# Kernel tuning notes

Hardware: AMD Instinct MI355X
Metric: run time of the kernel (lower is better)

## Reference

```python
import jax, jax.numpy as jnp
import numpy as np

EPS = float(np.finfo(np.float64).eps)


def _gat(x, src, dst, W, a_src, a_dst, b, N):
    # PyG GATConv, heads=1, concat=False, eval (no dropout). Self-loops already in src/dst.
    h = x @ W                              # [N, C]
    al = (h * a_src).sum(-1)               # [N] alpha_src per node
    ar = (h * a_dst).sum(-1)               # [N] alpha_dst per node
    e = jax.nn.leaky_relu(al[src] + ar[dst], 0.2)   # [E]
    m = jax.ops.segment_max(e, dst, num_segments=N)
    ee = jnp.exp(e - m[dst])
    s = jax.ops.segment_sum(ee, dst, num_segments=N)
    alpha = ee / (s[dst] + 1e-16)          # edge softmax grouped by dst
    return jax.ops.segment_sum(alpha[:, None] * h[src], dst, num_segments=N) + b


def setup_inputs() -> dict:
    key = jax.random.key(0)
    N, F, H, C, G, E = 10000, 128, 64, 2, 4, 320000
    ks = jax.random.split(key, 12)
    x = jax.random.normal(ks[0], (N, F), jnp.float32)
    y = jax.random.randint(ks[1], (N,), 0, 2)
    train_mask = jax.random.randint(ks[2], (N,), 0, 2).astype(jnp.int32)
    edge_ppi = jax.random.randint(ks[3], (2, E), 0, N)
    edge_hom = jax.random.randint(ks[4], (2, E), 0, N)
    g = lambda k, s, fan: jax.random.normal(k, s, jnp.float32) * (1.0 / np.sqrt(fan))
    W1 = g(ks[5], (G, F, H), F)
    a_src1 = g(ks[6], (G, H), H)
    a_dst1 = g(ks[7], (G, H), H)
    b1 = jnp.zeros((G, H), jnp.float32)
    gamma = jnp.ones((G, H), jnp.float32)
    beta = jnp.zeros((G, H), jnp.float32)
    W2 = g(ks[8], (G, H, C), H)
    a_src2 = g(ks[9], (G, C), C)
    a_dst2 = g(ks[10], (G, C), C)
    b2 = jnp.zeros((G, C), jnp.float32)
    emb_w = jnp.zeros((F,), jnp.float32)    # nn.Parameter init zeros
    logit_p = jnp.zeros((F,), jnp.float32)  # ConcreteDropout init zeros
    return dict(x=x, y=y, train_mask=train_mask, edge_ppi=edge_ppi, edge_hom=edge_hom,
                W1=W1, a_src1=a_src1, a_dst1=a_dst1, b1=b1, gamma=gamma, beta=beta,
                W2=W2, a_src2=a_src2, a_dst2=a_dst2, b2=b2, emb_w=emb_w, logit_p=logit_p)


def reference(x, y, train_mask, edge_ppi, edge_hom, W1, a_src1, a_dst1, b1,
              gamma, beta, W2, a_src2, a_dst2, b2, emb_w, logit_p):
    N = x.shape[0]
    G = W1.shape[0]
    loop = jnp.arange(N)
    sl = jnp.stack([loop, loop])
    ei_p = jnp.concatenate([edge_ppi, sl], axis=1)  # add self-loops (PyG default)
    ei_h = jnp.concatenate([edge_hom, sl], axis=1)
    mask = (train_mask > 0).astype(x.dtype)
    out = jnp.zeros((N,), x.dtype)
    loss = jnp.zeros((1,), x.dtype)
    for i in range(G):  # fixed small number of GAT branches
        ei = ei_p if i % 2 == 0 else ei_h
        src, dst = ei[0], ei[1]
        hid = _gat(x, src, dst, W1[i], a_src1[i], a_dst1[i], b1[i], N)
        hid = hid * gamma[i] / jnp.sqrt(1.0 + 1e-5) + beta[i]  # BN eval, init stats
        hid = jax.nn.leaky_relu(hid, 0.01)
        o = _gat(hid, src, dst, W2[i], a_src2[i], a_dst2[i], b2[i], N)
        logp = jax.nn.log_softmax(o, axis=1)
        pick = jnp.take_along_axis(logp, y[:, None], axis=1)[:, 0]
        loss = loss + (-(mask * pick).sum() / mask.sum())  # nll_loss on train_mask
        out = out + jnp.exp(logp[:, 1])
    node_p = out / G
    # GeneralizationGraph (eval: unif_noise = 0.5)
    p = jax.nn.sigmoid(logit_p)
    approx = (jnp.log(p + EPS) - jnp.log(1.0 - p + EPS)
              + jnp.log(0.5 + EPS) - jnp.log(0.5 + EPS))
    keep = 1.0 - jax.nn.sigmoid(approx / 0.1)
    emb = x * keep
    pw = 1.0 - p
    ex = emb * jax.nn.sigmoid(emb_w)
    graph = (ex @ ex.T) / (ex.sum(1) + 1e-6)  # [N,N]; column j scaled by 1/rowsum_j
    npc = node_p[:, None]
    adj = graph @ npc
    adj_n = graph @ (1.0 - npc)
    norm = jax.nn.softmax(jnp.concatenate([adj_n, adj], axis=1), axis=1)
    return (node_p, loss / G, norm[:, 1], graph, pw)
```

## Files before the change

### kernel.cpp

```cpp
#include <hip/hip_runtime.h>
#include <hip/hip_bf16.h>
#include <math.h>

#define N_NODES 10000
#define FDIM 128
#define HDIM 64
#define NEDGES 320000
#define M_EDGES (NEDGES + N_NODES)

typedef __attribute__((ext_vector_type(8))) short short8;
typedef __attribute__((ext_vector_type(4))) float floatx4;

__device__ __forceinline__ float lrelu(float v, float s){ return v >= 0.f ? v : s*v; }

__global__ void k_count(const int* __restrict__ ep, const int* __restrict__ eh,
                        int* __restrict__ ptr_p, int* __restrict__ ptr_h){
  int idx = blockIdx.x*blockDim.x + threadIdx.x;
  if (idx >= 2*M_EDGES) return;
  int list = idx >= M_EDGES;
  int e = idx - list*M_EDGES;
  const int* el = list ? eh : ep;
  int* ptr = list ? ptr_h : ptr_p;
  int dst = (e < NEDGES) ? el[NEDGES + e] : (e - NEDGES);
  atomicAdd(&ptr[dst+1], 1);
}

__global__ void k_scan(int* __restrict__ ptr_p, int* __restrict__ cur_p,
                       int* __restrict__ ptr_h, int* __restrict__ cur_h){
  __shared__ int wsum[4];
  __shared__ int carry;
  int t = threadIdx.x, wid = t>>6, lane = t&63;
  for (int a = 0; a < 2; ++a){
    int* ptr = a ? ptr_h : ptr_p;
    int* cur = a ? cur_h : cur_p;
    if (t == 0) carry = 0;
    __syncthreads();
    for (int base = 0; base <= N_NODES; base += 256){
      int i = base + t;
      int v = (i <= N_NODES) ? ptr[i] : 0;
      int sc = v;
      #pragma unroll
      for (int off=1; off<64; off<<=1){ int u = __shfl_up(sc, off); if (lane >= off) sc += u; }
      if (lane == 63) wsum[wid] = sc;
      __syncthreads();
      int wo = 0;
      for (int w = 0; w < wid; ++w) wo += wsum[w];
      int val = carry + wo + sc;
      if (i <= N_NODES) ptr[i] = val;
      if (i <  N_NODES) cur[i] = val;
      __syncthreads();
      if (t == 0) carry += wsum[0]+wsum[1]+wsum[2]+wsum[3];
      __syncthreads();
    }
  }
}

__global__ void k_fill(const int* __restrict__ ep, const int* __restrict__ eh,
                       int* __restrict__ cur_p, int* __restrict__ cur_h,
                       int* __restrict__ src_p, int* __restrict__ src_h){
  int idx = blockIdx.x*blockDim.x + threadIdx.x;
  if (idx >= 2*M_EDGES) return;
  int list = idx >= M_EDGES;
  int e = idx - list*M_EDGES;
  const int* el = list ? eh : ep;
  int* cur  = list ? cur_h : cur_p;
  int* sarr = list ? src_h : src_p;
  int src, dst;
  if (e < NEDGES){ src = el[e]; dst = el[NEDGES+e]; } else { src = dst = e - NEDGES; }
  int pos = atomicAdd(&cur[dst], 1);
  sarr[pos] = src;
}

__global__ void k_masksum(const int* __restrict__ tm, float* __restrict__ misc){
  __shared__ int ssum[4];
  int idx = blockIdx.x*blockDim.x + threadIdx.x;
  int c = 0;
  for (int i = idx; i < N_NODES; i += gridDim.x*blockDim.x) c += (tm[i] > 0);
  #pragma unroll
  for (int off=32; off; off>>=1) c += __shfl_down(c, off);
  if ((threadIdx.x & 63) == 0) ssum[threadIdx.x>>6] = c;
  __syncthreads();
  if (threadIdx.x == 0) atomicAdd(&misc[1], (float)(ssum[0]+ssum[1]+ssum[2]+ssum[3]));
}

__global__ __launch_bounds__(256) void k_gemm1(const float* __restrict__ x, const float* __restrict__ W1,
    const float* __restrict__ asrc, const float* __restrict__ adst,
    float* __restrict__ h, float* __restrict__ al, float* __restrict__ ar){
  int wid = threadIdx.x>>6, lane = threadIdx.x&63;
  int r = blockIdx.x*4 + wid;
  if (r >= N_NODES) return;
  const float* xr = x + (size_t)r*FDIM;
  float xv0 = xr[lane], xv1 = xr[64+lane];
  float acc = 0.f;
  #pragma unroll 16
  for (int k=0;k<64;k++) acc = fmaf(__shfl(xv0,k), W1[k*HDIM+lane], acc);
  #pragma unroll 16
  for (int k=0;k<64;k++) acc = fmaf(__shfl(xv1,k), W1[(64+k)*HDIM+lane], acc);
  h[(size_t)r*HDIM + lane] = acc;
  float pa = acc*asrc[lane], pb = acc*adst[lane];
  #pragma unroll
  for (int off=32; off; off>>=1){ pa += __shfl_down(pa,off); pb += __shfl_down(pb,off); }
  if (lane==0){ al[r]=pa; ar[r]=pb; }
}

__global__ __launch_bounds__(256) void k_gat1(const int* __restrict__ ptr, const int* __restrict__ srcarr,
    const float* __restrict__ al, const float* __restrict__ ar, const float* __restrict__ h,
    const float* __restrict__ b1, const float* __restrict__ gam, const float* __restrict__ bet,
    const float* __restrict__ W2, const float* __restrict__ asrc2, const float* __restrict__ adst2,
    float* __restrict__ h2, float* __restrict__ al2, float* __restrict__ ar2){
  int wid = threadIdx.x>>6, lane = threadIdx.x&63;
  int n = blockIdx.x*4 + wid;
  if (n >= N_NODES) return;
  int s0 = ptr[n], s1 = ptr[n+1];
  float arn = ar[n];
  float m_l = -3.0e38f, s_l = 0.f;
  for (int idx = s0+lane; idx < s1; idx += 64){
    int sj = srcarr[idx];
    float a = lrelu(al[sj]+arn, 0.2f);
    if (a > m_l){ s_l *= __expf(m_l - a); m_l = a; }
    s_l += __expf(a - m_l);
  }
  #pragma unroll
  for (int off=32; off; off>>=1){
    float mo = __shfl_down(m_l, off), so = __shfl_down(s_l, off);
    float mn = fmaxf(m_l, mo);
    s_l = s_l*__expf(m_l-mn) + so*__expf(mo-mn);
    m_l = mn;
  }
  float m = __shfl(m_l, 0);
  float inv_s = 1.f/(__shfl(s_l, 0) + 1e-16f);
  float acc = 0.f;
  for (int idx = s0; idx < s1; ++idx){
    int sj = srcarr[idx];
    float a = lrelu(al[sj]+arn, 0.2f);
    float w = __expf(a - m)*inv_s;
    acc = fmaf(w, h[(size_t)sj*HDIM + lane], acc);
  }
  float hid = acc + b1[lane];
  hid = hid*(gam[lane]*0.9999950000374997f) + bet[lane];
  hid = lrelu(hid, 0.01f);
  float t0 = hid*W2[lane*2+0], t1 = hid*W2[lane*2+1];
  #pragma unroll
  for (int off=32; off; off>>=1){ t0 += __shfl_down(t0,off); t1 += __shfl_down(t1,off); }
  if (lane==0){
    h2[n*2+0] = t0; h2[n*2+1] = t1;
    al2[n] = t0*asrc2[0] + t1*asrc2[1];
    ar2[n] = t0*adst2[0] + t1*adst2[1];
  }
}

__global__ __launch_bounds__(256) void k_gat2(const int* __restrict__ ptr, const int* __restrict__ srcarr,
    const float* __restrict__ al2, const float* __restrict__ ar2, const float* __restrict__ h2,
    const float* __restrict__ b2, const int* __restrict__ y, const int* __restrict__ tm,
    float* __restrict__ np_acc, float* __restrict__ misc){
  __shared__ float lbuf[4];
  int wid = threadIdx.x>>6, lane = threadIdx.x&63;
  int n = blockIdx.x*4 + wid;
  float lval = 0.f;
  if (n < N_NODES){
    int s0 = ptr[n], s1 = ptr[n+1];
    float arn = ar2[n];
    float m_l = -3.0e38f, s_l = 0.f;
    for (int idx = s0+lane; idx < s1; idx += 64){
      int sj = srcarr[idx];
      float a = lrelu(al2[sj]+arn, 0.2f);
      if (a > m_l){ s_l *= __expf(m_l - a); m_l = a; }
      s_l += __expf(a - m_l);
    }
    #pragma unroll
    for (int off=32; off; off>>=1){
      float mo = __shfl_down(m_l, off), so = __shfl_down(s_l, off);
      float mn = fmaxf(m_l, mo);
      s_l = s_l*__expf(m_l-mn) + so*__expf(mo-mn);
      m_l = mn;
    }
    float m = __shfl(m_l, 0);
    float sden = __shfl(s_l, 0) + 1e-16f;
    float a0 = 0.f, a1 = 0.f;
    for (int idx = s0+lane; idx < s1; idx += 64){
      int sj = srcarr[idx];
      float a = lrelu(al2[sj]+arn, 0.2f);
      float w = __expf(a - m);
      a0 = fmaf(w, h2[sj*2+0], a0);
      a1 = fmaf(w, h2[sj*2+1], a1);
    }
    #pragma unroll
    for (int off=32; off; off>>=1){ a0 += __shfl_down(a0,off); a1 += __shfl_down(a1,off); }
    if (lane == 0){
      float o0 = a0/sden + b2[0], o1 = a1/sden + b2[1];
      float mx = fmaxf(o0, o1);
      float lse = mx + logf(__expf(o0-mx) + __expf(o1-mx));
      float lp0 = o0 - lse, lp1 = o1 - lse;
      np_acc[n] += __expf(lp1);
      float pick = (y[n] == 0) ? lp0 : lp1;
      lval = (tm[n] > 0) ? -pick : 0.f;
    }
  }
  if (lane == 0) lbuf[wid] = lval;
  __syncthreads();
  if (threadIdx.x == 0){
    float tt = lbuf[0]+lbuf[1]+lbuf[2]+lbuf[3];
    atomicAdd(&misc[0], tt);
  }
}

__global__ void k_f(const float* __restrict__ logit_p, const float* __restrict__ emb_w,
                    float* __restrict__ keepsw, float* __restrict__ pw_out){
  int f = threadIdx.x;
  const float EPSF = 2.2204460492503131e-16f;
  float p = 1.f/(1.f + __expf(-logit_p[f]));
  float approx = logf(p + EPSF) - logf(1.f - p + EPSF);
  float keep = 1.f - 1.f/(1.f + __expf(-approx*10.f));
  keepsw[f] = keep * (1.f/(1.f + __expf(-emb_w[f])));
  pw_out[f] = 1.f - p;
}

__global__ __launch_bounds__(256) void k_ex(const float* __restrict__ x, const float* __restrict__ keepsw,
                                            __hip_bfloat16* __restrict__ exb, float* __restrict__ denom){
  int wid = threadIdx.x>>6, lane = threadIdx.x&63;
  int r = blockIdx.x*4 + wid;
  if (r >= N_NODES) return;
  const float* xr = x + (size_t)r*FDIM;
  float v0 = xr[lane]*keepsw[lane];
  float v1 = xr[64+lane]*keepsw[64+lane];
  exb[(size_t)r*FDIM + lane]      = __float2bfloat16(v0);
  exb[(size_t)r*FDIM + 64 + lane] = __float2bfloat16(v1);
  float sr = v0 + v1;
  #pragma unroll
  for (int off=32; off; off>>=1) sr += __shfl_down(sr, off);
  if (lane == 0) denom[r] = sr + 1e-6f;
}

__global__ void k_npfin(const float* __restrict__ np_acc, const float* __restrict__ denom,
                        const float* __restrict__ misc, float* __restrict__ out_np,
                        float* __restrict__ out_loss, float* __restrict__ scale){
  int i = blockIdx.x*blockDim.x + threadIdx.x;
  if (i < N_NODES){
    float npv = np_acc[i]*0.25f;
    out_np[i] = npv;
    scale[i] = (2.f*npv - 1.f)/denom[i];
  }
  if (i == 0) out_loss[0] = misc[0]/(misc[1]*4.f);
}

__global__ __launch_bounds__(256) void k_w2(const float* __restrict__ x, const float* __restrict__ keepsw,
                                            const float* __restrict__ scale, float* __restrict__ w2){
  __shared__ float sred[256];
  int t = threadIdx.x, f = t & 127, half = t >> 7;
  float acc = 0.f;
  for (int j2 = blockIdx.x; j2 < N_NODES/2; j2 += gridDim.x){
    int j = j2*2 + half;
    acc = fmaf(x[(size_t)j*FDIM + f], scale[j], acc);
  }
  sred[t] = acc;
  __syncthreads();
  if (t < 128) atomicAdd(&w2[f], (sred[t] + sred[t+128])*keepsw[f]);
}

__global__ __launch_bounds__(256) void k_t(const float* __restrict__ x, const float* __restrict__ keepsw,
                                           const float* __restrict__ w2, float* __restrict__ out_norm1){
  int wid = threadIdx.x>>6, lane = threadIdx.x&63;
  int r = blockIdx.x*4 + wid;
  if (r >= N_NODES) return;
  const float* xr = x + (size_t)r*FDIM;
  float tv = xr[lane]*keepsw[lane]*w2[lane] + xr[64+lane]*keepsw[64+lane]*w2[64+lane];
  #pragma unroll
  for (int off=32; off; off>>=1) tv += __shfl_down(tv, off);
  if (lane == 0) out_norm1[r] = 1.f/(1.f + __expf(-tv));
}

__global__ __launch_bounds__(256) void k_graph(const __hip_bfloat16* __restrict__ exb,
                                               const float* __restrict__ denom,
                                               float* __restrict__ gout){
  __shared__ ushort As[128*128];
  __shared__ ushort Bs[128*128];
  int t = threadIdx.x;
  int bi = blockIdx.y, bj = blockIdx.x;
  const ushort* exu = (const ushort*)exb;
  for (int it = 0; it < 8; ++it){
    int idx = it*256 + t;
    int r = idx >> 4;
    int c = idx & 15;
    int csw = c ^ (r & 15);
    int4 va = make_int4(0,0,0,0), vb = make_int4(0,0,0,0);
    int gi = bi*128 + r;
    int gj = bj*128 + r;
    if (gi < N_NODES) va = *(const int4*)(exu + (size_t)gi*FDIM + c*8);
    if (gj < N_NODES) vb = *(const int4*)(exu + (size_t)gj*FDIM + c*8);
    *(int4*)(&As[r*128 + csw*8]) = va;
    *(int4*)(&Bs[r*128 + csw*8]) = vb;
  }
  __syncthreads();
  int wid = t>>6, lane = t&63;
  int wy = wid>>1, wx = wid&1;
  int lr = lane&15, lq = lane>>4;
  floatx4 acc[4][4];
  #pragma unroll
  for (int a=0;a<4;a++)
    #pragma unroll
    for (int b=0;b<4;b++) acc[a][b] = (floatx4){0.f,0.f,0.f,0.f};
  #pragma unroll
  for (int ks = 0; ks < 4; ++ks){
    int cidx = ks*4 + lq;
    short8 af[4], bf[4];
    #pragma unroll
    for (int a=0;a<4;a++){
      int row = wy*64 + a*16 + lr;
      af[a] = *(const short8*)(&As[row*128 + (cidx ^ lr)*8]);
    }
    #pragma unroll
    for (int b=0;b<4;b++){
      int row = wx*64 + b*16 + lr;
      bf[b] = *(const short8*)(&Bs[row*128 + (cidx ^ lr)*8]);
    }
    #pragma unroll
    for (int a=0;a<4;a++)
      #pragma unroll
      for (int b=0;b<4;b++)
        acc[a][b] = __builtin_amdgcn_mfma_f32_16x16x32_bf16(af[a], bf[b], acc[a][b], 0, 0, 0);
  }
  #pragma unroll
  for (int b=0;b<4;b++){
    int j = bj*128 + wx*64 + b*16 + lr;
    float rden = (j < N_NODES) ? 1.f/denom[j] : 0.f;
    #pragma unroll
    for (int a=0;a<4;a++){
      int ibase = bi*128 + wy*64 + a*16 + lq*4;
      #pragma unroll
      for (int rr=0; rr<4; ++rr){
        int i = ibase + rr;
        if (i < N_NODES && j < N_NODES)
          gout[(size_t)i*N_NODES + j] = acc[a][b][rr]*rden;
      }
    }
  }
}

extern "C" void kernel_launch(void* const* d_in, const int* in_sizes, int n_in,
                              void* d_out, int out_size, void* d_ws, size_t ws_size,
                              hipStream_t stream) {
  (void)in_sizes; (void)n_in; (void)out_size;
  const float* x      = (const float*)d_in[0];
  const int*   y      = (const int*)  d_in[1];
  const int*   tmask  = (const int*)  d_in[2];
  const int*   ep     = (const int*)  d_in[3];
  const int*   eh     = (const int*)  d_in[4];
  const float* W1     = (const float*)d_in[5];
  const float* asrc1  = (const float*)d_in[6];
  const float* adst1  = (const float*)d_in[7];
  const float* b1     = (const float*)d_in[8];
  const float* gam    = (const float*)d_in[9];
  const float* bet    = (const float*)d_in[10];
  const float* W2     = (const float*)d_in[11];
  const float* asrc2  = (const float*)d_in[12];
  const float* adst2  = (const float*)d_in[13];
  const float* b2     = (const float*)d_in[14];
  const float* emb_w  = (const float*)d_in[15];
  const float* logitp = (const float*)d_in[16];

  constexpr size_t SZ_N4    = 40192;
  constexpr size_t OFF_PTR_P = 0;
  constexpr size_t OFF_PTR_H = OFF_PTR_P + SZ_N4;
  constexpr size_t OFF_NP    = OFF_PTR_H + SZ_N4;
  constexpr size_t OFF_MISC  = OFF_NP + SZ_N4;
  constexpr size_t ZBYTES    = OFF_MISC + 2048;
  constexpr size_t OFF_CUR_P = ZBYTES;
  constexpr size_t OFF_CUR_H = OFF_CUR_P + SZ_N4;
  constexpr size_t OFF_SRC_P = OFF_CUR_H + SZ_N4;
  constexpr size_t OFF_SRC_H = OFF_SRC_P + 1320192;
  constexpr size_t OFF_H     = OFF_SRC_H + 1320192;
  constexpr size_t OFF_AL    = OFF_H + 2560256;
  constexpr size_t OFF_AR    = OFF_AL + SZ_N4;
  constexpr size_t OFF_H2    = OFF_AR + SZ_N4;
  constexpr size_t OFF_AL2   = OFF_H2 + 80128;
  constexpr size_t OFF_AR2   = OFF_AL2 + SZ_N4;
  constexpr size_t OFF_EXB   = OFF_AR2 + SZ_N4;
  constexpr size_t OFF_DEN   = OFF_EXB + 2560256;
  constexpr size_t OFF_SCALE = OFF_DEN + SZ_N4;
  constexpr size_t OFF_KEEPSW= OFF_SCALE + SZ_N4;
  constexpr size_t WS_NEED   = OFF_KEEPSW + 512;
  if (ws_size < WS_NEED) return;

  char* ws = (char*)d_ws;
  int*   ptr_p  = (int*)  (ws + OFF_PTR_P);
  int*   ptr_h  = (int*)  (ws + OFF_PTR_H);
  float* np_acc = (float*)(ws + OFF_NP);
  float* misc   = (float*)(ws + OFF_MISC);
  float* w2v    = (float*)(ws + OFF_MISC + 256);
  int*   cur_p  = (int*)  (ws + OFF_CUR_P);
  int*   cur_h  = (int*)  (ws + OFF_CUR_H);
  int*   src_p  = (int*)  (ws + OFF_SRC_P);
  int*   src_h  = (int*)  (ws + OFF_SRC_H);
  float* hbuf   = (float*)(ws + OFF_H);
  float* al     = (float*)(ws + OFF_AL);
  float* ar     = (float*)(ws + OFF_AR);
  float* h2     = (float*)(ws + OFF_H2);
  float* al2    = (float*)(ws + OFF_AL2);
  float* ar2    = (float*)(ws + OFF_AR2);
  __hip_bfloat16* exb = (__hip_bfloat16*)(ws + OFF_EXB);
  float* denom  = (float*)(ws + OFF_DEN);
  float* scale  = (float*)(ws + OFF_SCALE);
  float* keepsw = (float*)(ws + OFF_KEEPSW);

  float* out       = (float*)d_out;
  float* out_np    = out;
  float* out_loss  = out + 10000;
  float* out_norm  = out + 10001;
  float* out_graph = out + 20001;
  float* out_pw    = out + 100020001;

  hipMemsetAsync(ws, 0, ZBYTES, stream);

  int eg = (2*M_EDGES + 255)/256;
  k_count<<<eg, 256, 0, stream>>>(ep, eh, ptr_p, ptr_h);
  k_scan<<<1, 256, 0, stream>>>(ptr_p, cur_p, ptr_h, cur_h);
  k_fill<<<eg, 256, 0, stream>>>(ep, eh, cur_p, cur_h, src_p, src_h);
  k_masksum<<<40, 256, 0, stream>>>(tmask, misc);

  for (int i = 0; i < 4; ++i){
    const int* ptr  = (i % 2 == 0) ? ptr_p : ptr_h;
    const int* sarr = (i % 2 == 0) ? src_p : src_h;
    k_gemm1<<<2500, 256, 0, stream>>>(x, W1 + (size_t)i*FDIM*HDIM, asrc1 + i*HDIM, adst1 + i*HDIM,
                                      hbuf, al, ar);
    k_gat1<<<2500, 256, 0, stream>>>(ptr, sarr, al, ar, hbuf,
                                     b1 + i*HDIM, gam + i*HDIM, bet + i*HDIM,
                                     W2 + (size_t)i*HDIM*2, asrc2 + i*2, adst2 + i*2,
                                     h2, al2, ar2);
    k_gat2<<<2500, 256, 0, stream>>>(ptr, sarr, al2, ar2, h2, b2 + i*2, y, tmask, np_acc, misc);
  }

  k_f<<<1, 128, 0, stream>>>(logitp, emb_w, keepsw, out_pw);
  k_ex<<<2500, 256, 0, stream>>>(x, keepsw, exb, denom);
  k_npfin<<<40, 256, 0, stream>>>(np_acc, denom, misc, out_np, out_loss, scale);
  k_w2<<<64, 256, 0, stream>>>(x, keepsw, scale, w2v);
  k_t<<<2500, 256, 0, stream>>>(x, keepsw, w2v, out_norm);

  dim3 gg((N_NODES + 127)/128, (N_NODES + 127)/128);
  k_graph<<<gg, 256, 0, stream>>>(exb, denom, out_graph);
}
```

Baseline: 1.115 ms.

## Batch the four GAT branches into single launches and fuse softmax passes

The per-branch loop of three GAT kernels becomes one launch per kernel, with the branch index taken from blockIdx.y and per-branch strided buffers. Per-node results are stored per branch and summed in k_npfin, replacing the accumulate into a shared array. Both GAT kernels now use a single-pass online softmax that rescales the running accumulators, removing the separate max/sum pass. k_gat1 also prefetches the next neighbour's feature row. Separately, the mask count moves into k_count, the feature-keep computation moves into k_ex, and the two CSR scans run as two blocks in parallel. The aim is fewer launches, more parallel work per launch and fewer passes over the edge lists, at the cost of a larger workspace.

```diff
diff --git a/kernel.cpp b/kernel.cpp
--- a/kernel.cpp
+++ b/kernel.cpp
@@ -11,11 +11,20 @@
 typedef __attribute__((ext_vector_type(8))) short short8;
 typedef __attribute__((ext_vector_type(4))) float floatx4;
 
+#define AL_STR 10048
+#define H_STR  640064
+#define H2_STR 20032
+
 __device__ __forceinline__ float lrelu(float v, float s){ return v >= 0.f ? v : s*v; }
 
 __global__ void k_count(const int* __restrict__ ep, const int* __restrict__ eh,
-                        int* __restrict__ ptr_p, int* __restrict__ ptr_h){
+                        int* __restrict__ ptr_p, int* __restrict__ ptr_h,
+                        const int* __restrict__ tm, float* __restrict__ misc){
   int idx = blockIdx.x*blockDim.x + threadIdx.x;
+  int c = (idx < N_NODES) ? (tm[idx] > 0) : 0;
+  #pragma unroll
+  for (int off=32; off; off>>=1) c += __shfl_down(c, off);
+  if ((threadIdx.x & 63) == 0 && c > 0) atomicAdd(&misc[1], (float)c);
   if (idx >= 2*M_EDGES) return;
   int list = idx >= M_EDGES;
   int e = idx - list*M_EDGES;
@@ -30,28 +39,26 @@
   __shared__ int wsum[4];
   __shared__ int carry;
   int t = threadIdx.x, wid = t>>6, lane = t&63;
-  for (int a = 0; a < 2; ++a){
-    int* ptr = a ? ptr_h : ptr_p;
-    int* cur = a ? cur_h : cur_p;
-    if (t == 0) carry = 0;
+  int* ptr = blockIdx.x ? ptr_h : ptr_p;
+  int* cur = blockIdx.x ? cur_h : cur_p;
+  if (t == 0) carry = 0;
+  __syncthreads();
+  for (int base = 0; base <= N_NODES; base += 256){
+    int i = base + t;
+    int v = (i <= N_NODES) ? ptr[i] : 0;
+    int sc = v;
+    #pragma unroll
+    for (int off=1; off<64; off<<=1){ int u = __shfl_up(sc, off); if (lane >= off) sc += u; }
+    if (lane == 63) wsum[wid] = sc;
     __syncthreads();
-    for (int base = 0; base <= N_NODES; base += 256){
-      int i = base + t;
-      int v = (i <= N_NODES) ? ptr[i] : 0;
-      int sc = v;
-      #pragma unroll
-      for (int off=1; off<64; off<<=1){ int u = __shfl_up(sc, off); if (lane >= off) sc += u; }
-      if (lane == 63) wsum[wid] = sc;
-      __syncthreads();
-      int wo = 0;
-      for (int w = 0; w < wid; ++w) wo += wsum[w];
-      int val = carry + wo + sc;
-      if (i <= N_NODES) ptr[i] = val;
-      if (i <  N_NODES) cur[i] = val;
-      __syncthreads();
-      if (t == 0) carry += wsum[0]+wsum[1]+wsum[2]+wsum[3];
-      __syncthreads();
-    }
+    int wo = 0;
+    for (int w = 0; w < wid; ++w) wo += wsum[w];
+    int val = carry + wo + sc;
+    if (i <= N_NODES) ptr[i] = val;
+    if (i <  N_NODES) cur[i] = val;
+    __syncthreads();
+    if (t == 0) carry += wsum[0]+wsum[1]+wsum[2]+wsum[3];
+    __syncthreads();
   }
 }
 
@@ -71,21 +78,16 @@
   sarr[pos] = src;
 }
 
-__global__ void k_masksum(const int* __restrict__ tm, float* __restrict__ misc){
-  __shared__ int ssum[4];
-  int idx = blockIdx.x*blockDim.x + threadIdx.x;
-  int c = 0;
-  for (int i = idx; i < N_NODES; i += gridDim.x*blockDim.x) c += (tm[i] > 0);
-  #pragma unroll
-  for (int off=32; off; off>>=1) c += __shfl_down(c, off);
-  if ((threadIdx.x & 63) == 0) ssum[threadIdx.x>>6] = c;
-  __syncthreads();
-  if (threadIdx.x == 0) atomicAdd(&misc[1], (float)(ssum[0]+ssum[1]+ssum[2]+ssum[3]));
-}
-
 __global__ __launch_bounds__(256) void k_gemm1(const float* __restrict__ x, const float* __restrict__ W1,
     const float* __restrict__ asrc, const float* __restrict__ adst,
     float* __restrict__ h, float* __restrict__ al, float* __restrict__ ar){
+  int l = blockIdx.y;
+  const float* W = W1 + (size_t)l*FDIM*HDIM;
+  const float* as = asrc + l*HDIM;
+  const float* ad = adst + l*HDIM;
+  float* hl  = h  + (size_t)l*H_STR;
+  float* all = al + (size_t)l*AL_STR;
+  float* arl = ar + (size_t)l*AL_STR;
   int wid = threadIdx.x>>6, lane = threadIdx.x&63;
   int r = blockIdx.x*4 + wid;
   if (r >= N_NODES) return;
@@ -93,105 +95,124 @@
   float xv0 = xr[lane], xv1 = xr[64+lane];
   float acc = 0.f;
   #pragma unroll 16
-  for (int k=0;k<64;k++) acc = fmaf(__shfl(xv0,k), W1[k*HDIM+lane], acc);
+  for (int k=0;k<64;k++) acc = fmaf(__shfl(xv0,k), W[k*HDIM+lane], acc);
   #pragma unroll 16
-  for (int k=0;k<64;k++) acc = fmaf(__shfl(xv1,k), W1[(64+k)*HDIM+lane], acc);
-  h[(size_t)r*HDIM + lane] = acc;
-  float pa = acc*asrc[lane], pb = acc*adst[lane];
+  for (int k=0;k<64;k++) acc = fmaf(__shfl(xv1,k), W[(64+k)*HDIM+lane], acc);
+  hl[(size_t)r*HDIM + lane] = acc;
+  float pa = acc*as[lane], pb = acc*ad[lane];
   #pragma unroll
   for (int off=32; off; off>>=1){ pa += __shfl_down(pa,off); pb += __shfl_down(pb,off); }
-  if (lane==0){ al[r]=pa; ar[r]=pb; }
-}
-
-__global__ __launch_bounds__(256) void k_gat1(const int* __restrict__ ptr, const int* __restrict__ srcarr,
+  if (lane==0){ all[r]=pa; arl[r]=pb; }
+}
+
+__global__ __launch_bounds__(256) void k_gat1(const int* __restrict__ ptr_p, const int* __restrict__ src_p,
+    const int* __restrict__ ptr_h, const int* __restrict__ src_h,
     const float* __restrict__ al, const float* __restrict__ ar, const float* __restrict__ h,
     const float* __restrict__ b1, const float* __restrict__ gam, const float* __restrict__ bet,
     const float* __restrict__ W2, const float* __restrict__ asrc2, const float* __restrict__ adst2,
     float* __restrict__ h2, float* __restrict__ al2, float* __restrict__ ar2){
+  int l = blockIdx.y;
+  const int* ptr    = (l & 1) ? ptr_h : ptr_p;
+  const int* srcarr = (l & 1) ? src_h : src_p;
+  const float* all = al + (size_t)l*AL_STR;
+  const float* arl = ar + (size_t)l*AL_STR;
+  const float* hl  = h  + (size_t)l*H_STR;
+  const float* b1l = b1 + l*HDIM;
+  const float* gl  = gam + l*HDIM;
+  const float* bl  = bet + l*HDIM;
+  const float* W   = W2 + (size_t)l*HDIM*2;
   int wid = threadIdx.x>>6, lane = threadIdx.x&63;
   int n = blockIdx.x*4 + wid;
   if (n >= N_NODES) return;
   int s0 = ptr[n], s1 = ptr[n+1];
-  float arn = ar[n];
-  float m_l = -3.0e38f, s_l = 0.f;
-  for (int idx = s0+lane; idx < s1; idx += 64){
-    int sj = srcarr[idx];
-    float a = lrelu(al[sj]+arn, 0.2f);
-    if (a > m_l){ s_l *= __expf(m_l - a); m_l = a; }
-    s_l += __expf(a - m_l);
-  }
-  #pragma unroll
-  for (int off=32; off; off>>=1){
-    float mo = __shfl_down(m_l, off), so = __shfl_down(s_l, off);
-    float mn = fmaxf(m_l, mo);
-    s_l = s_l*__expf(m_l-mn) + so*__expf(mo-mn);
-    m_l = mn;
-  }
-  float m = __shfl(m_l, 0);
-  float inv_s = 1.f/(__shfl(s_l, 0) + 1e-16f);
-  float acc = 0.f;
-  for (int idx = s0; idx < s1; ++idx){
-    int sj = srcarr[idx];
-    float a = lrelu(al[sj]+arn, 0.2f);
-    float w = __expf(a - m)*inv_s;
-    acc = fmaf(w, h[(size_t)sj*HDIM + lane], acc);
-  }
-  float hid = acc + b1[lane];
-  hid = hid*(gam[lane]*0.9999950000374997f) + bet[lane];
+  float arn = arl[n];
+  float m = -3.0e38f, s = 0.f, acc = 0.f;
+  for (int base = s0; base < s1; base += 64){
+    int cnt = min(64, s1 - base);
+    int sj = 0; float aval = -3.0e38f;
+    if (lane < cnt){ sj = srcarr[base + lane]; aval = lrelu(all[sj] + arn, 0.2f); }
+    float cm = aval;
+    #pragma unroll
+    for (int off=32; off; off>>=1) cm = fmaxf(cm, __shfl_xor(cm, off));
+    float mn = fmaxf(m, cm);
+    float r  = __expf(m - mn);
+    s *= r; acc *= r; m = mn;
+    int   sjt = __shfl(sj, 0);
+    float hv  = hl[(size_t)sjt*HDIM + lane];
+    for (int t = 0; t < cnt; ++t){
+      float a = __shfl(aval, t);
+      float w = __expf(a - m);
+      float hc = hv;
+      if (t + 1 < cnt){ int sn = __shfl(sj, t+1); hv = hl[(size_t)sn*HDIM + lane]; }
+      s  += (lane == 0) ? w : 0.f;
+      s  -= (lane == 0) ? 0.f : 0.f;
+      acc = fmaf(w, hc, acc);
+      if (lane != 0) s += w;
+    }
+  }
+  float hid = acc/(s + 1e-16f) + b1l[lane];
+  hid = hid*(gl[lane]*0.9999950000374997f) + bl[lane];
   hid = lrelu(hid, 0.01f);
-  float t0 = hid*W2[lane*2+0], t1 = hid*W2[lane*2+1];
+  float t0 = hid*W[lane*2+0], t1 = hid*W[lane*2+1];
   #pragma unroll
   for (int off=32; off; off>>=1){ t0 += __shfl_down(t0,off); t1 += __shfl_down(t1,off); }
   if (lane==0){
-    h2[n*2+0] = t0; h2[n*2+1] = t1;
-    al2[n] = t0*asrc2[0] + t1*asrc2[1];
-    ar2[n] = t0*adst2[0] + t1*adst2[1];
-  }
-}
-
-__global__ __launch_bounds__(256) void k_gat2(const int* __restrict__ ptr, const int* __restrict__ srcarr,
+    float* h2l = h2 + (size_t)l*H2_STR;
+    h2l[n*2+0] = t0; h2l[n*2+1] = t1;
+    al2[(size_t)l*AL_STR + n] = t0*asrc2[l*2+0] + t1*asrc2[l*2+1];
+    ar2[(size_t)l*AL_STR + n] = t0*adst2[l*2+0] + t1*adst2[l*2+1];
+  }
+}
+
+__global__ __launch_bounds__(256) void k_gat2(const int* __restrict__ ptr_p, const int* __restrict__ src_p,
+    const int* __restrict__ ptr_h, const int* __restrict__ src_h,
     const float* __restrict__ al2, const float* __restrict__ ar2, const float* __restrict__ h2,
     const float* __restrict__ b2, const int* __restrict__ y, const int* __restrict__ tm,
-    float* __restrict__ np_acc, float* __restrict__ misc){
+    float* __restrict__ np_arr, float* __restrict__ misc){
   __shared__ float lbuf[4];
+  int l = blockIdx.y;
+  const int* ptr    = (l & 1) ? ptr_h : ptr_p;
+  const int* srcarr = (l & 1) ? src_h : src_p;
+  const float* alL = al2 + (size_t)l*AL_STR;
+  const float* arL = ar2 + (size_t)l*AL_STR;
+  const float* h2l = h2  + (size_t)l*H2_STR;
   int wid = threadIdx.x>>6, lane = threadIdx.x&63;
   int n = blockIdx.x*4 + wid;
   float lval = 0.f;
   if (n < N_NODES){
     int s0 = ptr[n], s1 = ptr[n+1];
-    float arn = ar2[n];
-    float m_l = -3.0e38f, s_l = 0.f;
+    float arn = arL[n];
+    float m = -3.0e38f, s = 0.f, a0 = 0.f, a1 = 0.f;
     for (int idx = s0+lane; idx < s1; idx += 64){
       int sj = srcarr[idx];
-      float a = lrelu(al2[sj]+arn, 0.2f);
-      if (a > m_l){ s_l *= __expf(m_l - a); m_l = a; }
-      s_l += __expf(a - m_l);
+      float a = lrelu(alL[sj] + arn, 0.2f);
+      float2 hv = *(const float2*)(h2l + sj*2);
+      float mn = fmaxf(m, a);
+      float r  = __expf(m - mn);
+      float w  = __expf(a - mn);
+      s  = s*r + w;
+      a0 = a0*r + w*hv.x;
+      a1 = a1*r + w*hv.y;
+      m = mn;
     }
     #pragma unroll
     for (int off=32; off; off>>=1){
-      float mo = __shfl_down(m_l, off), so = __shfl_down(s_l, off);
-      float mn = fmaxf(m_l, mo);
-      s_l = s_l*__expf(m_l-mn) + so*__expf(mo-mn);
-      m_l = mn;
-    }
-    float m = __shfl(m_l, 0);
-    float sden = __shfl(s_l, 0) + 1e-16f;
-    float a0 = 0.f, a1 = 0.f;
-    for (int idx = s0+lane; idx < s1; idx += 64){
-      int sj = srcarr[idx];
-      float a = lrelu(al2[sj]+arn, 0.2f);
-      float w = __expf(a - m);
-      a0 = fmaf(w, h2[sj*2+0], a0);
-      a1 = fmaf(w, h2[sj*2+1], a1);
-    }
-    #pragma unroll
-    for (int off=32; off; off>>=1){ a0 += __shfl_down(a0,off); a1 += __shfl_down(a1,off); }
+      float mo = __shfl_xor(m, off), so = __shfl_xor(s, off);
+      float b0 = __shfl_xor(a0, off), b1v = __shfl_xor(a1, off);
+      float mn = fmaxf(m, mo);
+      float r1 = __expf(m - mn), r2 = __expf(mo - mn);
+      s  = s*r1 + so*r2;
+      a0 = a0*r1 + b0*r2;
+      a1 = a1*r1 + b1v*r2;
+      m = mn;
+    }
     if (lane == 0){
-      float o0 = a0/sden + b2[0], o1 = a1/sden + b2[1];
+      float sden = s + 1e-16f;
+      float o0 = a0/sden + b2[l*2+0], o1 = a1/sden + b2[l*2+1];
       float mx = fmaxf(o0, o1);
       float lse = mx + logf(__expf(o0-mx) + __expf(o1-mx));
       float lp0 = o0 - lse, lp1 = o1 - lse;
-      np_acc[n] += __expf(lp1);
+      np_arr[(size_t)l*AL_STR + n] = __expf(lp1);
       float pick = (y[n] == 0) ? lp0 : lp1;
       lval = (tm[n] > 0) ? -pick : 0.f;
     }
@@ -200,29 +221,32 @@
   __syncthreads();
   if (threadIdx.x == 0){
     float tt = lbuf[0]+lbuf[1]+lbuf[2]+lbuf[3];
-    atomicAdd(&misc[0], tt);
-  }
-}
-
-__global__ void k_f(const float* __restrict__ logit_p, const float* __restrict__ emb_w,
-                    float* __restrict__ keepsw, float* __restrict__ pw_out){
-  int f = threadIdx.x;
-  const float EPSF = 2.2204460492503131e-16f;
-  float p = 1.f/(1.f + __expf(-logit_p[f]));
-  float approx = logf(p + EPSF) - logf(1.f - p + EPSF);
-  float keep = 1.f - 1.f/(1.f + __expf(-approx*10.f));
-  keepsw[f] = keep * (1.f/(1.f + __expf(-emb_w[f])));
-  pw_out[f] = 1.f - p;
-}
-
-__global__ __launch_bounds__(256) void k_ex(const float* __restrict__ x, const float* __restrict__ keepsw,
-                                            __hip_bfloat16* __restrict__ exb, float* __restrict__ denom){
-  int wid = threadIdx.x>>6, lane = threadIdx.x&63;
+    if (tt != 0.f) atomicAdd(&misc[0], tt);
+  }
+}
+
+__global__ __launch_bounds__(256) void k_ex(const float* __restrict__ x,
+                                            const float* __restrict__ logit_p, const float* __restrict__ emb_w,
+                                            __hip_bfloat16* __restrict__ exb, float* __restrict__ denom,
+                                            float* __restrict__ keepsw, float* __restrict__ pw_out){
+  __shared__ float ksw[128];
+  int t = threadIdx.x;
+  if (t < 128){
+    const float EPSF = 2.2204460492503131e-16f;
+    float p = 1.f/(1.f + __expf(-logit_p[t]));
+    float approx = logf(p + EPSF) - logf(1.f - p + EPSF);
+    float keep = 1.f - 1.f/(1.f + __expf(-approx*10.f));
+    float v = keep * (1.f/(1.f + __expf(-emb_w[t])));
+    ksw[t] = v;
+    if (blockIdx.x == 0){ keepsw[t] = v; pw_out[t] = 1.f - p; }
+  }
+  __syncthreads();
+  int wid = t>>6, lane = t&63;
   int r = blockIdx.x*4 + wid;
   if (r >= N_NODES) return;
   const float* xr = x + (size_t)r*FDIM;
-  float v0 = xr[lane]*keepsw[lane];
-  float v1 = xr[64+lane]*keepsw[64+lane];
+  float v0 = xr[lane]*ksw[lane];
+  float v1 = xr[64+lane]*ksw[64+lane];
   exb[(size_t)r*FDIM + lane]      = __float2bfloat16(v0);
   exb[(size_t)r*FDIM + 64 + lane] = __float2bfloat16(v1);
   float sr = v0 + v1;
@@ -231,12 +255,12 @@
   if (lane == 0) denom[r] = sr + 1e-6f;
 }
 
-__global__ void k_npfin(const float* __restrict__ np_acc, const float* __restrict__ denom,
+__global__ void k_npfin(const float* __restrict__ np_arr, const float* __restrict__ denom,
                         const float* __restrict__ misc, float* __restrict__ out_np,
                         float* __restrict__ out_loss, float* __restrict__ scale){
   int i = blockIdx.x*blockDim.x + threadIdx.x;
   if (i < N_NODES){
-    float npv = np_acc[i]*0.25f;
+    float npv = 0.25f*(np_arr[i] + np_arr[AL_STR+i] + np_arr[2*AL_STR+i] + np_arr[3*AL_STR+i]);
     out_np[i] = npv;
     scale[i] = (2.f*npv - 1.f)/denom[i];
   }
@@ -358,35 +382,36 @@
   const float* emb_w  = (const float*)d_in[15];
   const float* logitp = (const float*)d_in[16];
 
-  constexpr size_t SZ_N4    = 40192;
+  constexpr size_t SZ_N4 = 40192;
   constexpr size_t OFF_PTR_P = 0;
   constexpr size_t OFF_PTR_H = OFF_PTR_P + SZ_N4;
-  constexpr size_t OFF_NP    = OFF_PTR_H + SZ_N4;
-  constexpr size_t OFF_MISC  = OFF_NP + SZ_N4;
-  constexpr size_t ZBYTES    = OFF_MISC + 2048;
+  constexpr size_t OFF_MISC  = OFF_PTR_H + SZ_N4;
+  constexpr size_t OFF_W2V   = OFF_MISC + 256;
+  constexpr size_t OFF_KSW   = OFF_MISC + 768;
+  constexpr size_t ZBYTES    = OFF_MISC + 1280;
   constexpr size_t OFF_CUR_P = ZBYTES;
   constexpr size_t OFF_CUR_H = OFF_CUR_P + SZ_N4;
   constexpr size_t OFF_SRC_P = OFF_CUR_H + SZ_N4;
   constexpr size_t OFF_SRC_H = OFF_SRC_P + 1320192;
   constexpr size_t OFF_H     = OFF_SRC_H + 1320192;
-  constexpr size_t OFF_AL    = OFF_H + 2560256;
-  constexpr size_t OFF_AR    = OFF_AL + SZ_N4;
-  constexpr size_t OFF_H2    = OFF_AR + SZ_N4;
-  constexpr size_t OFF_AL2   = OFF_H2 + 80128;
-  constexpr size_t OFF_AR2   = OFF_AL2 + SZ_N4;
-  constexpr size_t OFF_EXB   = OFF_AR2 + SZ_N4;
+  constexpr size_t OFF_AL    = OFF_H  + 4*(size_t)H_STR*4;
+  constexpr size_t OFF_AR    = OFF_AL + 4*SZ_N4;
+  constexpr size_t OFF_H2    = OFF_AR + 4*SZ_N4;
+  constexpr size_t OFF_AL2   = OFF_H2 + 4*(size_t)H2_STR*4;
+  constexpr size_t OFF_AR2   = OFF_AL2 + 4*SZ_N4;
+  constexpr size_t OFF_NP    = OFF_AR2 + 4*SZ_N4;
+  constexpr size_t OFF_EXB   = OFF_NP  + 4*SZ_N4;
   constexpr size_t OFF_DEN   = OFF_EXB + 2560256;
   constexpr size_t OFF_SCALE = OFF_DEN + SZ_N4;
-  constexpr size_t OFF_KEEPSW= OFF_SCALE + SZ_N4;
-  constexpr size_t WS_NEED   = OFF_KEEPSW + 512;
+  constexpr size_t WS_NEED   = OFF_SCALE + SZ_N4;
   if (ws_size < WS_NEED) return;
 
   char* ws = (char*)d_ws;
   int*   ptr_p  = (int*)  (ws + OFF_PTR_P);
   int*   ptr_h  = (int*)  (ws + OFF_PTR_H);
-  float* np_acc = (float*)(ws + OFF_NP);
   float* misc   = (float*)(ws + OFF_MISC);
-  float* w2v    = (float*)(ws + OFF_MISC + 256);
+  float* w2v    = (float*)(ws + OFF_W2V);
+  float* keepsw = (float*)(ws + OFF_KSW);
   int*   cur_p  = (int*)  (ws + OFF_CUR_P);
   int*   cur_h  = (int*)  (ws + OFF_CUR_H);
   int*   src_p  = (int*)  (ws + OFF_SRC_P);
@@ -397,10 +422,10 @@
   float* h2     = (float*)(ws + OFF_H2);
   float* al2    = (float*)(ws + OFF_AL2);
   float* ar2    = (float*)(ws + OFF_AR2);
+  float* np_arr = (float*)(ws + OFF_NP);
   __hip_bfloat16* exb = (__hip_bfloat16*)(ws + OFF_EXB);
   float* denom  = (float*)(ws + OFF_DEN);
   float* scale  = (float*)(ws + OFF_SCALE);
-  float* keepsw = (float*)(ws + OFF_KEEPSW);
 
   float* out       = (float*)d_out;
   float* out_np    = out;
@@ -412,26 +437,19 @@
   hipMemsetAsync(ws, 0, ZBYTES, stream);
 
   int eg = (2*M_EDGES + 255)/256;
-  k_count<<<eg, 256, 0, stream>>>(ep, eh, ptr_p, ptr_h);
-  k_scan<<<1, 256, 0, stream>>>(ptr_p, cur_p, ptr_h, cur_h);
+  k_count<<<eg, 256, 0, stream>>>(ep, eh, ptr_p, ptr_h, tmask, misc);
+  k_scan<<<2, 256, 0, stream>>>(ptr_p, cur_p, ptr_h, cur_h);
   k_fill<<<eg, 256, 0, stream>>>(ep, eh, cur_p, cur_h, src_p, src_h);
-  k_masksum<<<40, 256, 0, stream>>>(tmask, misc);
-
-  for (int i = 0; i < 4; ++i){
-    const int* ptr  = (i % 2 == 0) ? ptr_p : ptr_h;
-    const int* sarr = (i % 2 == 0) ? src_p : src_h;
-    k_gemm1<<<2500, 256, 0, stream>>>(x, W1 + (size_t)i*FDIM*HDIM, asrc1 + i*HDIM, adst1 + i*HDIM,
-                                      hbuf, al, ar);
-    k_gat1<<<2500, 256, 0, stream>>>(ptr, sarr, al, ar, hbuf,
-                                     b1 + i*HDIM, gam + i*HDIM, bet + i*HDIM,
-                                     W2 + (size_t)i*HDIM*2, asrc2 + i*2, adst2 + i*2,
-                                     h2, al2, ar2);
-    k_gat2<<<2500, 256, 0, stream>>>(ptr, sarr, al2, ar2, h2, b2 + i*2, y, tmask, np_acc, misc);
-  }
-
-  k_f<<<1, 128, 0, stream>>>(logitp, emb_w, keepsw, out_pw);
-  k_ex<<<2500, 256, 0, stream>>>(x, keepsw, exb, denom);
-  k_npfin<<<40, 256, 0, stream>>>(np_acc, denom, misc, out_np, out_loss, scale);
+
+  dim3 lg(2500, 4);
+  k_gemm1<<<lg, 256, 0, stream>>>(x, W1, asrc1, adst1, hbuf, al, ar);
+  k_gat1<<<lg, 256, 0, stream>>>(ptr_p, src_p, ptr_h, src_h, al, ar, hbuf,
+                                 b1, gam, bet, W2, asrc2, adst2, h2, al2, ar2);
+  k_gat2<<<lg, 256, 0, stream>>>(ptr_p, src_p, ptr_h, src_h, al2, ar2, h2,
+                                 b2, y, tmask, np_arr, misc);
+
+  k_ex<<<2500, 256, 0, stream>>>(x, logitp, emb_w, exb, denom, keepsw, out_pw);
+  k_npfin<<<40, 256, 0, stream>>>(np_arr, denom, misc, out_np, out_loss, scale);
   k_w2<<<64, 256, 0, stream>>>(x, keepsw, scale, w2v);
   k_t<<<2500, 256, 0, stream>>>(x, keepsw, w2v, out_norm);
 
```

Measured after the change: 984.5 us. 1.13x faster.
